# Kernel tuning notes

Hardware: AMD Instinct MI355X
Metric: run time of the kernel (lower is better)

Reference implementation:

```python
import jax, jax.numpy as jnp
import numpy as np

N, E, F, H, ED, C, G = 50000, 800000, 86, 128, 16, 18, 64
NEG_SLOPE = 0.2


def setup_inputs() -> dict:
    key = jax.random.key(0)
    ks = jax.random.split(key, 20)
    s = 0.1
    return {
        "x": jax.random.normal(ks[0], (N, F), jnp.float32),
        "edge_index": jax.random.randint(ks[1], (2, E), 0, N, jnp.int32),
        "edge_attr": jax.random.normal(ks[2], (E, ED), jnp.float32),
        "batch": jnp.sort(jax.random.randint(ks[3], (N,), 0, G, jnp.int32)),
        # conv1 params (GATConv, heads=1): lin, lin_edge (no bias), att vectors, bias
        "W1": jax.random.normal(ks[4], (F, H), jnp.float32) * s,
        "We1": jax.random.normal(ks[5], (ED, H), jnp.float32) * s,
        "as1": jax.random.normal(ks[6], (H,), jnp.float32) * s,
        "ad1": jax.random.normal(ks[7], (H,), jnp.float32) * s,
        "ae1": jax.random.normal(ks[8], (H,), jnp.float32) * s,
        "b1": jnp.zeros((H,), jnp.float32),
        # conv2 params
        "W2": jax.random.normal(ks[9], (H, H), jnp.float32) * s,
        "We2": jax.random.normal(ks[10], (ED, H), jnp.float32) * s,
        "as2": jax.random.normal(ks[11], (H,), jnp.float32) * s,
        "ad2": jax.random.normal(ks[12], (H,), jnp.float32) * s,
        "ae2": jax.random.normal(ks[13], (H,), jnp.float32) * s,
        "b2": jnp.zeros((H,), jnp.float32),
        # final classifier
        "Wl": jax.random.normal(ks[14], (H, C), jnp.float32) * s,
        "bl": jnp.zeros((C,), jnp.float32),
    }


def gat_conv(x, edge_attr, src, dst, W, We, a_src, a_dst, a_edge, bias):
    h = x @ W                                   # [N, H]
    e = edge_attr @ We                          # [E, H]
    # per-edge attention logits: a_src.h_j + a_dst.h_i + a_edge.e
    alpha = (h @ a_src)[src] + (h @ a_dst)[dst] + e @ a_edge   # [E]
    alpha = jax.nn.leaky_relu(alpha, NEG_SLOPE)
    # segment softmax over incoming edges of each destination node
    m = jax.ops.segment_max(alpha, dst, num_segments=N)
    ex = jnp.exp(alpha - m[dst])
    denom = jax.ops.segment_sum(ex, dst, num_segments=N)
    w = ex / jnp.maximum(denom[dst], 1e-16)     # [E]
    out = jax.ops.segment_sum(h[src] * w[:, None], dst, num_segments=N)
    return out + bias


def reference(x, edge_index, edge_attr, batch,
              W1, We1, as1, ad1, ae1, b1,
              W2, We2, as2, ad2, ae2, b2,
              Wl, bl):
    src, dst = edge_index[0], edge_index[1]
    h = jax.nn.relu(gat_conv(x, edge_attr, src, dst, W1, We1, as1, ad1, ae1, b1))
    h = jax.nn.relu(gat_conv(h, edge_attr, src, dst, W2, We2, as2, ad2, ae2, b2))
    pooled = jax.ops.segment_max(h, batch, num_segments=G)      # [G, H] global max pool
    pooled = jnp.where(jnp.isfinite(pooled), pooled, 0.0)       # guard empty graphs
    logits = pooled @ Wl + bl                                   # [G, C]
    return jax.nn.log_softmax(logits, axis=-1)
```

## Files before the change

### kernel.cpp

```cpp
#include <hip/hip_runtime.h>
#include <math.h>

#define N_NODES 50000
#define N_EDGES 800000
#define F_IN    86
#define H_DIM   128
#define ED_DIM  16
#define C_CLS   18
#define G_GRAPHS 64
#define NEG_SLOPE 0.2f
#define SCAN_BLOCKS ((N_NODES + 255) / 256)
#define EB_BLOCKS ((N_EDGES + 255) / 256)
#define GB_BLOCKS ((N_NODES + 63) / 64)
#define HB_BLOCKS 782
#define HB_THREADS (HB_BLOCKS * 256)

typedef _Float16 h2v   __attribute__((ext_vector_type(2)));
typedef _Float16 half8 __attribute__((ext_vector_type(8)));
typedef float    f4v   __attribute__((ext_vector_type(4)));
typedef unsigned long long ull;

__device__ __forceinline__ void atomicMaxFloat(float* addr, float val) {
    if (val >= 0.0f) atomicMax((int*)addr, __float_as_int(val));
    else             atomicMin((unsigned int*)addr, __float_as_uint(val));
}

__global__ void prep(int* __restrict__ cnt, float* __restrict__ pooled,
                     const float* __restrict__ We1, const float* __restrict__ ae1,
                     const float* __restrict__ We2, const float* __restrict__ ae2,
                     float* __restrict__ ve1, float* __restrict__ ve2,
                     const float* __restrict__ W1, const float* __restrict__ W2,
                     _Float16* __restrict__ w1t, _Float16* __restrict__ w2t) {
    int b = blockIdx.x, t = threadIdx.x;
    if (b < SCAN_BLOCKS) {
        int i = b * 256 + t;
        if (i < N_NODES) cnt[i] = 0;
    } else if (b == SCAN_BLOCKS) {
        if (t < ED_DIM) {
            float s = 0.f;
            for (int h = 0; h < H_DIM; ++h) s += We1[t * H_DIM + h] * ae1[h];
            ve1[t] = s;
        } else if (t < 2 * ED_DIM) {
            int j = t - ED_DIM;
            float s = 0.f;
            for (int h = 0; h < H_DIM; ++h) s += We2[j * H_DIM + h] * ae2[h];
            ve2[j] = s;
        }
        for (int i = t; i < G_GRAPHS * H_DIM; i += 256) pooled[i] = 0.f;
    } else if (b == SCAN_BLOCKS + 1) {
        for (int i = t; i < H_DIM * 96; i += 256) {
            int n = i / 96, k = i - n * 96;
            w1t[i] = (k < F_IN) ? (_Float16)W1[k * H_DIM + n] : (_Float16)0.f;
        }
    } else {
        for (int i = t; i < H_DIM * H_DIM; i += 256) {
            int n = i >> 7, k = i & 127;
            w2t[i] = (_Float16)W2[k * H_DIM + n];
        }
    }
}

__global__ void scan1(const int* __restrict__ cnt, int* __restrict__ excl,
                      int* __restrict__ bsum) {
    __shared__ int s[256];
    int tid = threadIdx.x;
    int i = blockIdx.x * 256 + tid;
    int v = (i < N_NODES) ? cnt[i] : 0;
    s[tid] = v;
    __syncthreads();
    for (int o = 1; o < 256; o <<= 1) {
        int t = (tid >= o) ? s[tid - o] : 0;
        __syncthreads();
        s[tid] += t;
        __syncthreads();
    }
    if (i < N_NODES) excl[i] = s[tid] - v;
    if (tid == 255) bsum[blockIdx.x] = s[255];
}

__global__ void scan23(const int* __restrict__ excl, const int* __restrict__ bsum,
                       int* __restrict__ row_ptr) {
    __shared__ int s[256];
    int tid = threadIdx.x;
    int v = (tid < SCAN_BLOCKS) ? bsum[tid] : 0;
    s[tid] = v;
    __syncthreads();
    for (int o = 1; o < 256; o <<= 1) {
        int t = (tid >= o) ? s[tid - o] : 0;
        __syncthreads();
        s[tid] += t;
        __syncthreads();
    }
    int boff = s[blockIdx.x] - bsum[blockIdx.x];
    int i = blockIdx.x * 256 + tid;
    if (i < N_NODES) row_ptr[i] = excl[i] + boff;
    if (i == 0) row_ptr[N_NODES] = N_EDGES;
}

__global__ void scatter_lite(const int* __restrict__ src, const int* __restrict__ dst,
                             const int* __restrict__ row_ptr,
                             const unsigned short* __restrict__ rank,
                             const unsigned int* __restrict__ dotp,
                             int2* __restrict__ perm) {
    int e = blockIdx.x * blockDim.x + threadIdx.x;
    if (e >= N_EDGES) return;
    int pos = row_ptr[dst[e]] + rank[e];
    perm[pos] = make_int2(src[e], (int)dotp[e]);
}

#define KP1 104
__global__ __launch_bounds__(256)
void gemm1_hist(const float* __restrict__ in, const _Float16* __restrict__ w1t,
                const float* __restrict__ a_s, const float* __restrict__ a_d,
                _Float16* __restrict__ hout, float* __restrict__ hs, float* __restrict__ hd,
                const int* __restrict__ dst, int* __restrict__ cnt,
                unsigned short* __restrict__ rank, const float* __restrict__ ea,
                const float* __restrict__ ve1, const float* __restrict__ ve2,
                unsigned int* __restrict__ dotp) {
    __shared__ __attribute__((aligned(16))) _Float16 Asm[64 * KP1];
    __shared__ float sdots[64][2][2];
    int tid = threadIdx.x;

    if (blockIdx.x >= GB_BLOCKS) {
        int tbase = (blockIdx.x - GB_BLOCKS) * 256 + tid;
#pragma unroll
        for (int u = 0; u < 4; ++u) {
            int e = tbase + u * HB_THREADS;
            if (e < N_EDGES) {
                int r = atomicAdd(&cnt[dst[e]], 1);
                rank[e] = (unsigned short)r;
                const float4* p = (const float4*)(ea + (size_t)e * ED_DIM);
                float4 v0 = p[0], v1 = p[1], v2 = p[2], v3 = p[3];
                float s1 = v0.x*ve1[0] + v0.y*ve1[1] + v0.z*ve1[2] + v0.w*ve1[3]
                         + v1.x*ve1[4] + v1.y*ve1[5] + v1.z*ve1[6] + v1.w*ve1[7]
                         + v2.x*ve1[8] + v2.y*ve1[9] + v2.z*ve1[10] + v2.w*ve1[11]
                         + v3.x*ve1[12] + v3.y*ve1[13] + v3.z*ve1[14] + v3.w*ve1[15];
                float s2 = v0.x*ve2[0] + v0.y*ve2[1] + v0.z*ve2[2] + v0.w*ve2[3]
                         + v1.x*ve2[4] + v1.y*ve2[5] + v1.z*ve2[6] + v1.w*ve2[7]
                         + v2.x*ve2[8] + v2.y*ve2[9] + v2.z*ve2[10] + v2.w*ve2[11]
                         + v3.x*ve2[12] + v3.y*ve2[13] + v3.z*ve2[14] + v3.w*ve2[15];
                h2v dv;
                dv.x = (_Float16)s1;
                dv.y = (_Float16)s2;
                dotp[e] = __builtin_bit_cast(unsigned int, dv);
            }
        }
        return;
    }

    int n0 = blockIdx.x * 64;
    const float2* in2 = (const float2*)(in + (size_t)n0 * F_IN);
    for (int idx = tid; idx < 64 * (F_IN / 2); idx += 256) {
        int r = idx / (F_IN / 2), k2 = idx - r * (F_IN / 2);
        float2 v = (n0 + r < N_NODES) ? in2[idx] : make_float2(0.f, 0.f);
        Asm[r * KP1 + 2 * k2]     = (_Float16)v.x;
        Asm[r * KP1 + 2 * k2 + 1] = (_Float16)v.y;
    }
    for (int idx = tid; idx < 64 * (96 - F_IN); idx += 256) {
        int r = idx / (96 - F_IN), k = F_IN + idx - r * (96 - F_IN);
        Asm[r * KP1 + k] = (_Float16)0.f;
    }
    __syncthreads();

    int wave = tid >> 6, lane = tid & 63;
    int wm = (wave & 1) * 32, wn = (wave >> 1) * 64;
    int m16 = lane & 15, quad = lane >> 4;

    f4v acc[2][4];
#pragma unroll
    for (int t = 0; t < 2; ++t)
#pragma unroll
        for (int c = 0; c < 4; ++c) acc[t][c] = (f4v){0.f, 0.f, 0.f, 0.f};

#pragma unroll
    for (int kk = 0; kk < 96 / 32; ++kk) {
        int koff = kk * 32 + quad * 8;
        half8 a0 = *(const half8*)&Asm[(wm + m16) * KP1 + koff];
        half8 a1 = *(const half8*)&Asm[(wm + 16 + m16) * KP1 + koff];
#pragma unroll
        for (int c = 0; c < 4; ++c) {
            half8 b = *(const half8*)&w1t[(wn + c * 16 + m16) * 96 + koff];
            acc[0][c] = __builtin_amdgcn_mfma_f32_16x16x32_f16(a0, b, acc[0][c], 0, 0, 0);
            acc[1][c] = __builtin_amdgcn_mfma_f32_16x16x32_f16(a1, b, acc[1][c], 0, 0, 0);
        }
    }

    float asv[4], adv[4];
#pragma unroll
    for (int c = 0; c < 4; ++c) {
        asv[c] = a_s[wn + c * 16 + m16];
        adv[c] = a_d[wn + c * 16 + m16];
    }
#pragma unroll
    for (int t = 0; t < 2; ++t)
#pragma unroll
        for (int r = 0; r < 4; ++r) {
            float ps = 0.f, pd = 0.f;
#pragma unroll
            for (int c = 0; c < 4; ++c) {
                float v = acc[t][c][r];
                ps += v * asv[c];
                pd += v * adv[c];
            }
#pragma unroll
            for (int o = 1; o < 16; o <<= 1) {
                ps += __shfl_xor(ps, o);
                pd += __shfl_xor(pd, o);
            }
            if (m16 == 0) {
                int row = wm + t * 16 + quad * 4 + r;
                sdots[row][wn >> 6][0] = ps;
                sdots[row][wn >> 6][1] = pd;
            }
        }
#pragma unroll
    for (int t = 0; t < 2; ++t)
#pragma unroll
        for (int c = 0; c < 4; ++c)
#pragma unroll
            for (int r = 0; r < 4; ++r) {
                int row = n0 + wm + t * 16 + quad * 4 + r;
                if (row < N_NODES)
                    hout[(size_t)row * H_DIM + wn + c * 16 + m16] = (_Float16)acc[t][c][r];
            }
    __syncthreads();
    if (tid < 64) {
        int row = n0 + tid;
        if (row < N_NODES) {
            hs[row] = sdots[tid][0][0] + sdots[tid][1][0];
            hd[row] = sdots[tid][0][1] + sdots[tid][1][1];
        }
    }
}

#define KP2 136
__global__ __launch_bounds__(256)
void gemm2(const _Float16* __restrict__ in, const _Float16* __restrict__ w2t,
           const float* __restrict__ a_s, const float* __restrict__ a_d,
           _Float16* __restrict__ hout, float* __restrict__ hs, float* __restrict__ hd) {
    __shared__ __attribute__((aligned(16))) _Float16 Asm[64 * KP2];
    __shared__ float sdots[64][2][2];
    int tid = threadIdx.x;
    int n0 = blockIdx.x * 64;

    const half8* in8 = (const half8*)(in + (size_t)n0 * H_DIM);
    for (int idx = tid; idx < 64 * 16; idx += 256) {
        int r = idx >> 4, k8 = idx & 15;
        half8 v = (n0 + r < N_NODES) ? in8[idx]
                                     : (half8){0, 0, 0, 0, 0, 0, 0, 0};
        *(half8*)&Asm[r * KP2 + k8 * 8] = v;
    }
    __syncthreads();

    int wave = tid >> 6, lane = tid & 63;
    int wm = (wave & 1) * 32, wn = (wave >> 1) * 64;
    int m16 = lane & 15, quad = lane >> 4;

    f4v acc[2][4];
#pragma unroll
    for (int t = 0; t < 2; ++t)
#pragma unroll
        for (int c = 0; c < 4; ++c) acc[t][c] = (f4v){0.f, 0.f, 0.f, 0.f};

#pragma unroll
    for (int kk = 0; kk < 128 / 32; ++kk) {
        int koff = kk * 32 + quad * 8;
        half8 a0 = *(const half8*)&Asm[(wm + m16) * KP2 + koff];
        half8 a1 = *(const half8*)&Asm[(wm + 16 + m16) * KP2 + koff];
#pragma unroll
        for (int c = 0; c < 4; ++c) {
            half8 b = *(const half8*)&w2t[(wn + c * 16 + m16) * H_DIM + koff];
            acc[0][c] = __builtin_amdgcn_mfma_f32_16x16x32_f16(a0, b, acc[0][c], 0, 0, 0);
            acc[1][c] = __builtin_amdgcn_mfma_f32_16x16x32_f16(a1, b, acc[1][c], 0, 0, 0);
        }
    }

    float asv[4], adv[4];
#pragma unroll
    for (int c = 0; c < 4; ++c) {
        asv[c] = a_s[wn + c * 16 + m16];
        adv[c] = a_d[wn + c * 16 + m16];
    }
#pragma unroll
    for (int t = 0; t < 2; ++t)
#pragma unroll
        for (int r = 0; r < 4; ++r) {
            float ps = 0.f, pd = 0.f;
#pragma unroll
            for (int c = 0; c < 4; ++c) {
                float v = acc[t][c][r];
                ps += v * asv[c];
                pd += v * adv[c];
            }
#pragma unroll
            for (int o = 1; o < 16; o <<= 1) {
                ps += __shfl_xor(ps, o);
                pd += __shfl_xor(pd, o);
            }
            if (m16 == 0) {
                int row = wm + t * 16 + quad * 4 + r;
                sdots[row][wn >> 6][0] = ps;
                sdots[row][wn >> 6][1] = pd;
            }
        }
#pragma unroll
    for (int t = 0; t < 2; ++t)
#pragma unroll
        for (int c = 0; c < 4; ++c)
#pragma unroll
            for (int r = 0; r < 4; ++r) {
                int row = n0 + wm + t * 16 + quad * 4 + r;
                if (row < N_NODES)
                    hout[(size_t)row * H_DIM + wn + c * 16 + m16] = (_Float16)acc[t][c][r];
            }
    __syncthreads();
    if (tid < 64) {
        int row = n0 + tid;
        if (row < N_NODES) {
            hs[row] = sdots[tid][0][0] + sdots[tid][1][0];
            hd[row] = sdots[tid][0][1] + sdots[tid][1][1];
        }
    }
}

template<int DOT, bool POOL>
__global__ void gat_node(const int* __restrict__ row_ptr, const int2* __restrict__ perm,
                         const float* __restrict__ hs, const float* __restrict__ hd,
                         const _Float16* __restrict__ h, const float* __restrict__ bias,
                         _Float16* __restrict__ out,
                         const int* __restrict__ batch, float* __restrict__ pooled) {
    __shared__ float smax[H_DIM];
    __shared__ int sg[4];
    __shared__ __attribute__((aligned(16))) ull stage[4][64];
    int tid = threadIdx.x;
    if (POOL) {
        if (tid < H_DIM) smax[tid] = 0.f;
        __syncthreads();
    }
    int n = blockIdx.x * 4 + (tid >> 6);
    int lane = tid & 63;
    int q = lane >> 4, m = lane & 15;
    int r0 = row_ptr[n], r1 = row_ptr[n + 1];
    float hdn = hd[n];
    const char* hb = (const char*)h;
    unsigned mo = (unsigned)(m * 16);
    ull* st = stage[tid >> 6];

    float acc[8];
#pragma unroll
    for (int k = 0; k < 8; ++k) acc[k] = 0.f;
    float denl = 0.f;

    for (int c = r0; c < r1; c += 64) {
        int i = c + lane;
        float w = 0.f;
        int so = 0;
        if (i < r1) {
            int2 p = perm[i];
            so = p.x * (H_DIM * 2);
            h2v dv = __builtin_bit_cast(h2v, p.y);
            float dotv = (DOT == 1) ? (float)dv.x : (float)dv.y;
            float t = hs[p.x] + hdn + dotv;
            t = (t > 0.f) ? t : NEG_SLOPE * t;
            w = __expf(t);
        }
        denl += w;
        st[lane] = (ull)(unsigned)so | ((ull)__float_as_uint(w) << 32);
        int lim = r1 - c; if (lim > 64) lim = 64;
        int njj = (lim + 7) >> 3;
        int jj = 0;
        for (; jj + 2 <= njj; jj += 2) {
            int b8 = jj << 3;
            ull p1 = st[b8 + q];
            ull p2 = st[b8 + q + 4];
            ull p3 = st[b8 + q + 8];
            ull p4 = st[b8 + q + 12];
            float w1 = __uint_as_float((unsigned)(p1 >> 32));
            float w2 = __uint_as_float((unsigned)(p2 >> 32));
            float w3 = __uint_as_float((unsigned)(p3 >> 32));
            float w4 = __uint_as_float((unsigned)(p4 >> 32));
            half8 v1 = *(const half8*)(hb + ((unsigned)p1 + mo));
            half8 v2 = *(const half8*)(hb + ((unsigned)p2 + mo));
            half8 v3 = *(const half8*)(hb + ((unsigned)p3 + mo));
            half8 v4 = *(const half8*)(hb + ((unsigned)p4 + mo));
#pragma unroll
            for (int k = 0; k < 8; ++k) acc[k] += w1 * (float)v1[k];
#pragma unroll
            for (int k = 0; k < 8; ++k) acc[k] += w2 * (float)v2[k];
#pragma unroll
            for (int k = 0; k < 8; ++k) acc[k] += w3 * (float)v3[k];
#pragma unroll
            for (int k = 0; k < 8; ++k) acc[k] += w4 * (float)v4[k];
        }
        if (jj < njj) {
            int b8 = jj << 3;
            ull p1 = st[b8 + q];
            ull p2 = st[b8 + q + 4];
            float w1 = __uint_as_float((unsigned)(p1 >> 32));
            float w2 = __uint_as_float((unsigned)(p2 >> 32));
            half8 v1 = *(const half8*)(hb + ((unsigned)p1 + mo));
            half8 v2 = *(const half8*)(hb + ((unsigned)p2 + mo));
#pragma unroll
            for (int k = 0; k < 8; ++k) acc[k] += w1 * (float)v1[k];
#pragma unroll
            for (int k = 0; k < 8; ++k) acc[k] += w2 * (float)v2[k];
        }
    }
#pragma unroll
    for (int k = 0; k < 8; ++k) {
        acc[k] += __shfl_xor(acc[k], 16);
        acc[k] += __shfl_xor(acc[k], 32);
    }
    float den = denl;
#pragma unroll
    for (int o = 32; o > 0; o >>= 1) den += __shfl_xor(den, o);
    float inv = 1.f / fmaxf(den, 1e-16f);

    float rv[8];
    if (q == 0) {
        float4 b0 = ((const float4*)bias)[2 * m];
        float4 b1 = ((const float4*)bias)[2 * m + 1];
        rv[0] = fmaxf(acc[0] * inv + b0.x, 0.f);
        rv[1] = fmaxf(acc[1] * inv + b0.y, 0.f);
        rv[2] = fmaxf(acc[2] * inv + b0.z, 0.f);
        rv[3] = fmaxf(acc[3] * inv + b0.w, 0.f);
        rv[4] = fmaxf(acc[4] * inv + b1.x, 0.f);
        rv[5] = fmaxf(acc[5] * inv + b1.y, 0.f);
        rv[6] = fmaxf(acc[6] * inv + b1.z, 0.f);
        rv[7] = fmaxf(acc[7] * inv + b1.w, 0.f);
    }

    if (!POOL) {
        if (q == 0) {
            half8 ov;
#pragma unroll
            for (int k = 0; k < 8; ++k) ov[k] = (_Float16)rv[k];
            *(half8*)&out[(size_t)n * H_DIM + m * 8] = ov;
        }
    } else {
        int g = batch[n];
        if (lane == 0) sg[tid >> 6] = g;
        if (q == 0) {
#pragma unroll
            for (int k = 0; k < 8; ++k)
                atomicMax((int*)&smax[m * 8 + k], __float_as_int(rv[k]));
        }
        __syncthreads();
        if (sg[0] == sg[3]) {
            if (tid < H_DIM)
                atomicMaxFloat(&pooled[sg[0] * H_DIM + tid], smax[tid]);
        } else {
            if (q == 0) {
#pragma unroll
                for (int k = 0; k < 8; ++k)
                    atomicMaxFloat(&pooled[g * H_DIM + m * 8 + k], rv[k]);
            }
        }
    }
}

__global__ void final_logits(const float* __restrict__ pooled, const float* __restrict__ Wl,
                             const float* __restrict__ bl, float* __restrict__ outp) {
    int g = threadIdx.x;
    if (g >= G_GRAPHS) return;
    float lg[C_CLS];
#pragma unroll
    for (int c = 0; c < C_CLS; ++c) lg[c] = bl[c];
    for (int k = 0; k < H_DIM; ++k) {
        float v = pooled[g * H_DIM + k];
#pragma unroll
        for (int c = 0; c < C_CLS; ++c) lg[c] += v * Wl[k * C_CLS + c];
    }
    float mx = lg[0];
#pragma unroll
    for (int c = 1; c < C_CLS; ++c) mx = fmaxf(mx, lg[c]);
    float se = 0.f;
#pragma unroll
    for (int c = 0; c < C_CLS; ++c) se += expf(lg[c] - mx);
    float lse = logf(se);
#pragma unroll
    for (int c = 0; c < C_CLS; ++c) outp[g * C_CLS + c] = lg[c] - mx - lse;
}

extern "C" void kernel_launch(void* const* d_in, const int* in_sizes, int n_in,
                              void* d_out, int out_size, void* d_ws, size_t ws_size,
                              hipStream_t stream) {
    const float* x     = (const float*)d_in[0];
    const int*   eidx  = (const int*)d_in[1];
    const float* ea    = (const float*)d_in[2];
    const int*   batch = (const int*)d_in[3];
    const float* W1  = (const float*)d_in[4];
    const float* We1 = (const float*)d_in[5];
    const float* as1 = (const float*)d_in[6];
    const float* ad1 = (const float*)d_in[7];
    const float* ae1 = (const float*)d_in[8];
    const float* b1  = (const float*)d_in[9];
    const float* W2  = (const float*)d_in[10];
    const float* We2 = (const float*)d_in[11];
    const float* as2 = (const float*)d_in[12];
    const float* ad2 = (const float*)d_in[13];
    const float* ae2 = (const float*)d_in[14];
    const float* b2  = (const float*)d_in[15];
    const float* Wl  = (const float*)d_in[16];
    const float* bl  = (const float*)d_in[17];
    float* outp = (float*)d_out;

    const int* src = eidx;
    const int* dst = eidx + N_EDGES;

    char* wsb = (char*)d_ws;
    size_t off = 0;
    auto alloc = [&](size_t bytes) { char* p = wsb + off; off += (bytes + 255) & ~(size_t)255; return p; };
    _Float16* h    = (_Float16*)alloc((size_t)N_NODES * H_DIM * 2);
    _Float16* A2   = (_Float16*)alloc((size_t)N_NODES * H_DIM * 2);
    int2*  perm    = (int2*)alloc((size_t)N_EDGES * 8);
    unsigned short* rank = (unsigned short*)alloc((size_t)N_EDGES * 2);
    unsigned int* dotp = (unsigned int*)alloc((size_t)N_EDGES * 4);
    float* hs      = (float*)alloc(N_NODES * 4);
    float* hd      = (float*)alloc(N_NODES * 4);
    int*   row_ptr = (int*)alloc((N_NODES + 1) * 4);
    int*   cnt     = (int*)alloc(N_NODES * 4);
    int*   excl    = (int*)alloc(N_NODES * 4);
    int*   bsum    = (int*)alloc(SCAN_BLOCKS * 4);
    float* pooled  = (float*)alloc(G_GRAPHS * H_DIM * 4);
    float* ve1     = (float*)alloc(16 * 4);
    float* ve2     = (float*)alloc(16 * 4);
    _Float16* w1t  = (_Float16*)alloc(H_DIM * 96 * 2);
    _Float16* w2t  = (_Float16*)alloc(H_DIM * H_DIM * 2);

    const int NB4 = (N_NODES + 3) / 4;

    prep<<<SCAN_BLOCKS + 3, 256, 0, stream>>>(cnt, pooled, We1, ae1, We2, ae2, ve1, ve2,
                                              W1, W2, w1t, w2t);
    gemm1_hist<<<GB_BLOCKS + HB_BLOCKS, 256, 0, stream>>>(x, w1t, as1, ad1, h, hs, hd,
                                                          dst, cnt, rank, ea, ve1, ve2, dotp);
    scan1<<<SCAN_BLOCKS, 256, 0, stream>>>(cnt, excl, bsum);
    scan23<<<SCAN_BLOCKS, 256, 0, stream>>>(excl, bsum, row_ptr);
    scatter_lite<<<EB_BLOCKS, 256, 0, stream>>>(src, dst, row_ptr, rank, dotp, perm);

    gat_node<1, false><<<NB4, 256, 0, stream>>>(row_ptr, perm, hs, hd, h, b1, A2,
                                                batch, pooled);

    gemm2<<<GB_BLOCKS, 256, 0, stream>>>(A2, w2t, as2, ad2, h, hs, hd);
    gat_node<2, true><<<NB4, 256, 0, stream>>>(row_ptr, perm, hs, hd, h, b2, nullptr,
                                               batch, pooled);

    final_logits<<<1, 64, 0, stream>>>(pooled, Wl, bl, outp);
}
```

Before: 305.6 us.

## Merge edge histogram into GEMM blocks and fuse scan offset with CSR scatter

The edge histogram, rank and edge-attribute dot products are now done inside every GEMM1 block rather than in separate trailing blocks. The atomics are issued early so their latency can overlap the MFMA work, and the weight fragments are hoisted into registers. The second scan pass and the CSR scatter become one kernel that recomputes block offsets in shared memory, which removes a launch and the dependency on row_ptr. In exchange, GEMM blocks carry more register pressure and the scan work is repeated in every one of the 3125 scatter blocks.

After: 310.1 us. No clear change (+1.5%).

```diff
diff --git a/kernel.cpp b/kernel.cpp
--- a/kernel.cpp
+++ b/kernel.cpp
@@ -12,8 +12,7 @@
 #define SCAN_BLOCKS ((N_NODES + 255) / 256)
 #define EB_BLOCKS ((N_EDGES + 255) / 256)
 #define GB_BLOCKS ((N_NODES + 63) / 64)
-#define HB_BLOCKS 782
-#define HB_THREADS (HB_BLOCKS * 256)
+#define HB_THREADS (GB_BLOCKS * 256)
 
 typedef _Float16 h2v   __attribute__((ext_vector_type(2)));
 typedef _Float16 half8 __attribute__((ext_vector_type(8)));
@@ -78,8 +77,12 @@
     if (tid == 255) bsum[blockIdx.x] = s[255];
 }
 
-__global__ void scan23(const int* __restrict__ excl, const int* __restrict__ bsum,
-                       int* __restrict__ row_ptr) {
+__global__ void scan_scatter(const int* __restrict__ excl, const int* __restrict__ bsum,
+                             int* __restrict__ row_ptr,
+                             const int* __restrict__ src, const int* __restrict__ dst,
+                             const unsigned short* __restrict__ rank,
+                             const unsigned int* __restrict__ dotp,
+                             int2* __restrict__ perm) {
     __shared__ int s[256];
     int tid = threadIdx.x;
     int v = (tid < SCAN_BLOCKS) ? bsum[tid] : 0;
@@ -91,21 +94,20 @@
         s[tid] += t;
         __syncthreads();
     }
-    int boff = s[blockIdx.x] - bsum[blockIdx.x];
-    int i = blockIdx.x * 256 + tid;
-    if (i < N_NODES) row_ptr[i] = excl[i] + boff;
-    if (i == 0) row_ptr[N_NODES] = N_EDGES;
-}
-
-__global__ void scatter_lite(const int* __restrict__ src, const int* __restrict__ dst,
-                             const int* __restrict__ row_ptr,
-                             const unsigned short* __restrict__ rank,
-                             const unsigned int* __restrict__ dotp,
-                             int2* __restrict__ perm) {
-    int e = blockIdx.x * blockDim.x + threadIdx.x;
-    if (e >= N_EDGES) return;
-    int pos = row_ptr[dst[e]] + rank[e];
-    perm[pos] = make_int2(src[e], (int)dotp[e]);
+    int eb = s[tid] - v;
+    __syncthreads();
+    s[tid] = eb;
+    __syncthreads();
+    int e = blockIdx.x * 256 + tid;
+    if (blockIdx.x < SCAN_BLOCKS) {
+        if (e < N_NODES) row_ptr[e] = excl[e] + s[e >> 8];
+        if (e == 0) row_ptr[N_NODES] = N_EDGES;
+    }
+    if (e < N_EDGES) {
+        int d = dst[e];
+        int pos = excl[d] + s[d >> 8] + rank[e];
+        perm[pos] = make_int2(src[e], (int)dotp[e]);
+    }
 }
 
 #define KP1 104
@@ -120,35 +122,9 @@
     __shared__ __attribute__((aligned(16))) _Float16 Asm[64 * KP1];
     __shared__ float sdots[64][2][2];
     int tid = threadIdx.x;
-
-    if (blockIdx.x >= GB_BLOCKS) {
-        int tbase = (blockIdx.x - GB_BLOCKS) * 256 + tid;
-#pragma unroll
-        for (int u = 0; u < 4; ++u) {
-            int e = tbase + u * HB_THREADS;
-            if (e < N_EDGES) {
-                int r = atomicAdd(&cnt[dst[e]], 1);
-                rank[e] = (unsigned short)r;
-                const float4* p = (const float4*)(ea + (size_t)e * ED_DIM);
-                float4 v0 = p[0], v1 = p[1], v2 = p[2], v3 = p[3];
-                float s1 = v0.x*ve1[0] + v0.y*ve1[1] + v0.z*ve1[2] + v0.w*ve1[3]
-                         + v1.x*ve1[4] + v1.y*ve1[5] + v1.z*ve1[6] + v1.w*ve1[7]
-                         + v2.x*ve1[8] + v2.y*ve1[9] + v2.z*ve1[10] + v2.w*ve1[11]
-                         + v3.x*ve1[12] + v3.y*ve1[13] + v3.z*ve1[14] + v3.w*ve1[15];
-                float s2 = v0.x*ve2[0] + v0.y*ve2[1] + v0.z*ve2[2] + v0.w*ve2[3]
-                         + v1.x*ve2[4] + v1.y*ve2[5] + v1.z*ve2[6] + v1.w*ve2[7]
-                         + v2.x*ve2[8] + v2.y*ve2[9] + v2.z*ve2[10] + v2.w*ve2[11]
-                         + v3.x*ve2[12] + v3.y*ve2[13] + v3.z*ve2[14] + v3.w*ve2[15];
-                h2v dv;
-                dv.x = (_Float16)s1;
-                dv.y = (_Float16)s2;
-                dotp[e] = __builtin_bit_cast(unsigned int, dv);
-            }
-        }
-        return;
-    }
-
     int n0 = blockIdx.x * 64;
+    int e0 = blockIdx.x * 256 + tid;
+
     const float2* in2 = (const float2*)(in + (size_t)n0 * F_IN);
     for (int idx = tid; idx < 64 * (F_IN / 2); idx += 256) {
         int r = idx / (F_IN / 2), k2 = idx - r * (F_IN / 2);
@@ -166,31 +142,43 @@
     int wm = (wave & 1) * 32, wn = (wave >> 1) * 64;
     int m16 = lane & 15, quad = lane >> 4;
 
+    half8 bf[3][4];
+#pragma unroll
+    for (int kk = 0; kk < 3; ++kk)
+#pragma unroll
+        for (int c = 0; c < 4; ++c)
+            bf[kk][c] = *(const half8*)&w1t[(wn + c * 16 + m16) * 96 + kk * 32 + quad * 8];
+    float asv[4], adv[4];
+#pragma unroll
+    for (int c = 0; c < 4; ++c) {
+        asv[c] = a_s[wn + c * 16 + m16];
+        adv[c] = a_d[wn + c * 16 + m16];
+    }
+
+    int rv4[4];
+#pragma unroll
+    for (int u = 0; u < 4; ++u) {
+        int e = e0 + u * HB_THREADS;
+        rv4[u] = (e < N_EDGES) ? atomicAdd(&cnt[dst[e]], 1) : 0;
+    }
+
     f4v acc[2][4];
 #pragma unroll
     for (int t = 0; t < 2; ++t)
 #pragma unroll
         for (int c = 0; c < 4; ++c) acc[t][c] = (f4v){0.f, 0.f, 0.f, 0.f};
-
-#pragma unroll
-    for (int kk = 0; kk < 96 / 32; ++kk) {
+#pragma unroll
+    for (int kk = 0; kk < 3; ++kk) {
         int koff = kk * 32 + quad * 8;
         half8 a0 = *(const half8*)&Asm[(wm + m16) * KP1 + koff];
         half8 a1 = *(const half8*)&Asm[(wm + 16 + m16) * KP1 + koff];
 #pragma unroll
         for (int c = 0; c < 4; ++c) {
-            half8 b = *(const half8*)&w1t[(wn + c * 16 + m16) * 96 + koff];
-            acc[0][c] = __builtin_amdgcn_mfma_f32_16x16x32_f16(a0, b, acc[0][c], 0, 0, 0);
-            acc[1][c] = __builtin_amdgcn_mfma_f32_16x16x32_f16(a1, b, acc[1][c], 0, 0, 0);
-        }
-    }
-
-    float asv[4], adv[4];
-#pragma unroll
-    for (int c = 0; c < 4; ++c) {
-        asv[c] = a_s[wn + c * 16 + m16];
-        adv[c] = a_d[wn + c * 16 + m16];
-    }
+            acc[0][c] = __builtin_amdgcn_mfma_f32_16x16x32_f16(a0, bf[kk][c], acc[0][c], 0, 0, 0);
+            acc[1][c] = __builtin_amdgcn_mfma_f32_16x16x32_f16(a1, bf[kk][c], acc[1][c], 0, 0, 0);
+        }
+    }
+
 #pragma unroll
     for (int t = 0; t < 2; ++t)
 #pragma unroll
@@ -223,6 +211,28 @@
                 if (row < N_NODES)
                     hout[(size_t)row * H_DIM + wn + c * 16 + m16] = (_Float16)acc[t][c][r];
             }
+
+#pragma unroll
+    for (int u = 0; u < 4; ++u) {
+        int e = e0 + u * HB_THREADS;
+        if (e < N_EDGES) {
+            rank[e] = (unsigned short)rv4[u];
+            const float4* p = (const float4*)(ea + (size_t)e * ED_DIM);
+            float4 v0 = p[0], v1 = p[1], v2 = p[2], v3 = p[3];
+            float s1 = v0.x*ve1[0] + v0.y*ve1[1] + v0.z*ve1[2] + v0.w*ve1[3]
+                     + v1.x*ve1[4] + v1.y*ve1[5] + v1.z*ve1[6] + v1.w*ve1[7]
+                     + v2.x*ve1[8] + v2.y*ve1[9] + v2.z*ve1[10] + v2.w*ve1[11]
+                     + v3.x*ve1[12] + v3.y*ve1[13] + v3.z*ve1[14] + v3.w*ve1[15];
+            float s2 = v0.x*ve2[0] + v0.y*ve2[1] + v0.z*ve2[2] + v0.w*ve2[3]
+                     + v1.x*ve2[4] + v1.y*ve2[5] + v1.z*ve2[6] + v1.w*ve2[7]
+                     + v2.x*ve2[8] + v2.y*ve2[9] + v2.z*ve2[10] + v2.w*ve2[11]
+                     + v3.x*ve2[12] + v3.y*ve2[13] + v3.z*ve2[14] + v3.w*ve2[15];
+            h2v dv;
+            dv.x = (_Float16)s1;
+            dv.y = (_Float16)s2;
+            dotp[e] = __builtin_bit_cast(unsigned int, dv);
+        }
+    }
     __syncthreads();
     if (tid < 64) {
         int row = n0 + tid;
@@ -532,11 +542,11 @@
 
     prep<<<SCAN_BLOCKS + 3, 256, 0, stream>>>(cnt, pooled, We1, ae1, We2, ae2, ve1, ve2,
                                               W1, W2, w1t, w2t);
-    gemm1_hist<<<GB_BLOCKS + HB_BLOCKS, 256, 0, stream>>>(x, w1t, as1, ad1, h, hs, hd,
-                                                          dst, cnt, rank, ea, ve1, ve2, dotp);
+    gemm1_hist<<<GB_BLOCKS, 256, 0, stream>>>(x, w1t, as1, ad1, h, hs, hd,
+                                              dst, cnt, rank, ea, ve1, ve2, dotp);
     scan1<<<SCAN_BLOCKS, 256, 0, stream>>>(cnt, excl, bsum);
-    scan23<<<SCAN_BLOCKS, 256, 0, stream>>>(excl, bsum, row_ptr);
-    scatter_lite<<<EB_BLOCKS, 256, 0, stream>>>(src, dst, row_ptr, rank, dotp, perm);
+    scan_scatter<<<EB_BLOCKS, 256, 0, stream>>>(excl, bsum, row_ptr, src, dst,
+                                                rank, dotp, perm);
 
     gat_node<1, false><<<NB4, 256, 0, stream>>>(row_ptr, perm, hs, hd, h, b1, A2,
                                                 batch, pooled);
```

## Split histogram counters into two banks and fuse scan offsets with edge scatter

Applied to the files above, without the earlier changes.

The per-destination atomic histogram is split into two counter arrays chosen by edge parity, which halves contention on hot counters. The scan-add and scatter kernels are merged into one launch that recomputes block offsets in each block and writes perm directly. The edge-attribute dot products move from the histogram kernel into the scatter, so the dotp intermediate array and its round trip through memory are gone. In exchange, every scatter block redoes the block-sum scan, each edge reads more (excl, cnt0, edge attributes), and an extra counter array must be zeroed and read.

Result: no change. 310.8 us (+1.7%).

```diff
diff --git a/kernel.cpp b/kernel.cpp
--- a/kernel.cpp
+++ b/kernel.cpp
@@ -25,7 +25,8 @@
     else             atomicMin((unsigned int*)addr, __float_as_uint(val));
 }
 
-__global__ void prep(int* __restrict__ cnt, float* __restrict__ pooled,
+__global__ void prep(int* __restrict__ cnt0, int* __restrict__ cnt1,
+                     float* __restrict__ pooled,
                      const float* __restrict__ We1, const float* __restrict__ ae1,
                      const float* __restrict__ We2, const float* __restrict__ ae2,
                      float* __restrict__ ve1, float* __restrict__ ve2,
@@ -34,7 +35,7 @@
     int b = blockIdx.x, t = threadIdx.x;
     if (b < SCAN_BLOCKS) {
         int i = b * 256 + t;
-        if (i < N_NODES) cnt[i] = 0;
+        if (i < N_NODES) { cnt0[i] = 0; cnt1[i] = 0; }
     } else if (b == SCAN_BLOCKS) {
         if (t < ED_DIM) {
             float s = 0.f;
@@ -60,12 +61,12 @@
     }
 }
 
-__global__ void scan1(const int* __restrict__ cnt, int* __restrict__ excl,
-                      int* __restrict__ bsum) {
+__global__ void scan1(const int* __restrict__ cnt0, const int* __restrict__ cnt1,
+                      int* __restrict__ excl, int* __restrict__ bsum) {
     __shared__ int s[256];
     int tid = threadIdx.x;
     int i = blockIdx.x * 256 + tid;
-    int v = (i < N_NODES) ? cnt[i] : 0;
+    int v = (i < N_NODES) ? cnt0[i] + cnt1[i] : 0;
     s[tid] = v;
     __syncthreads();
     for (int o = 1; o < 256; o <<= 1) {
@@ -78,8 +79,14 @@
     if (tid == 255) bsum[blockIdx.x] = s[255];
 }
 
-__global__ void scan23(const int* __restrict__ excl, const int* __restrict__ bsum,
-                       int* __restrict__ row_ptr) {
+__global__ void scan_scatter(const int* __restrict__ excl, const int* __restrict__ bsum,
+                             int* __restrict__ row_ptr,
+                             const int* __restrict__ src, const int* __restrict__ dst,
+                             const unsigned short* __restrict__ rank,
+                             const int* __restrict__ cnt0,
+                             const float* __restrict__ ea,
+                             const float* __restrict__ ve1, const float* __restrict__ ve2,
+                             int2* __restrict__ perm) {
     __shared__ int s[256];
     int tid = threadIdx.x;
     int v = (tid < SCAN_BLOCKS) ? bsum[tid] : 0;
@@ -91,21 +98,35 @@
         s[tid] += t;
         __syncthreads();
     }
-    int boff = s[blockIdx.x] - bsum[blockIdx.x];
-    int i = blockIdx.x * 256 + tid;
-    if (i < N_NODES) row_ptr[i] = excl[i] + boff;
-    if (i == 0) row_ptr[N_NODES] = N_EDGES;
-}
-
-__global__ void scatter_lite(const int* __restrict__ src, const int* __restrict__ dst,
-                             const int* __restrict__ row_ptr,
-                             const unsigned short* __restrict__ rank,
-                             const unsigned int* __restrict__ dotp,
-                             int2* __restrict__ perm) {
-    int e = blockIdx.x * blockDim.x + threadIdx.x;
-    if (e >= N_EDGES) return;
-    int pos = row_ptr[dst[e]] + rank[e];
-    perm[pos] = make_int2(src[e], (int)dotp[e]);
+    int eb = s[tid] - v;
+    __syncthreads();
+    s[tid] = eb;
+    __syncthreads();
+    int e = blockIdx.x * 256 + tid;
+    if (blockIdx.x < SCAN_BLOCKS) {
+        if (e < N_NODES) row_ptr[e] = excl[e] + s[e >> 8];
+        if (e == 0) row_ptr[N_NODES] = N_EDGES;
+    }
+    if (e < N_EDGES) {
+        int d = dst[e];
+        int base = excl[d] + s[d >> 8];
+        int off = (e & 1) ? cnt0[d] : 0;
+        int pos = base + off + rank[e];
+        const float4* p = (const float4*)(ea + (size_t)e * ED_DIM);
+        float4 v0 = p[0], v1 = p[1], v2 = p[2], v3 = p[3];
+        float s1 = v0.x*ve1[0] + v0.y*ve1[1] + v0.z*ve1[2] + v0.w*ve1[3]
+                 + v1.x*ve1[4] + v1.y*ve1[5] + v1.z*ve1[6] + v1.w*ve1[7]
+                 + v2.x*ve1[8] + v2.y*ve1[9] + v2.z*ve1[10] + v2.w*ve1[11]
+                 + v3.x*ve1[12] + v3.y*ve1[13] + v3.z*ve1[14] + v3.w*ve1[15];
+        float s2 = v0.x*ve2[0] + v0.y*ve2[1] + v0.z*ve2[2] + v0.w*ve2[3]
+                 + v1.x*ve2[4] + v1.y*ve2[5] + v1.z*ve2[6] + v1.w*ve2[7]
+                 + v2.x*ve2[8] + v2.y*ve2[9] + v2.z*ve2[10] + v2.w*ve2[11]
+                 + v3.x*ve2[12] + v3.y*ve2[13] + v3.z*ve2[14] + v3.w*ve2[15];
+        h2v dv;
+        dv.x = (_Float16)s1;
+        dv.y = (_Float16)s2;
+        perm[pos] = make_int2(src[e], (int)__builtin_bit_cast(unsigned int, dv));
+    }
 }
 
 #define KP1 104
@@ -113,36 +134,21 @@
 void gemm1_hist(const float* __restrict__ in, const _Float16* __restrict__ w1t,
                 const float* __restrict__ a_s, const float* __restrict__ a_d,
                 _Float16* __restrict__ hout, float* __restrict__ hs, float* __restrict__ hd,
-                const int* __restrict__ dst, int* __restrict__ cnt,
-                unsigned short* __restrict__ rank, const float* __restrict__ ea,
-                const float* __restrict__ ve1, const float* __restrict__ ve2,
-                unsigned int* __restrict__ dotp) {
+                const int* __restrict__ dst, int* __restrict__ cnt0, int* __restrict__ cnt1,
+                unsigned short* __restrict__ rank) {
     __shared__ __attribute__((aligned(16))) _Float16 Asm[64 * KP1];
     __shared__ float sdots[64][2][2];
     int tid = threadIdx.x;
 
     if (blockIdx.x >= GB_BLOCKS) {
         int tbase = (blockIdx.x - GB_BLOCKS) * 256 + tid;
+        int* bank = (tbase & 1) ? cnt1 : cnt0;
 #pragma unroll
         for (int u = 0; u < 4; ++u) {
             int e = tbase + u * HB_THREADS;
             if (e < N_EDGES) {
-                int r = atomicAdd(&cnt[dst[e]], 1);
+                int r = atomicAdd(&bank[dst[e]], 1);
                 rank[e] = (unsigned short)r;
-                const float4* p = (const float4*)(ea + (size_t)e * ED_DIM);
-                float4 v0 = p[0], v1 = p[1], v2 = p[2], v3 = p[3];
-                float s1 = v0.x*ve1[0] + v0.y*ve1[1] + v0.z*ve1[2] + v0.w*ve1[3]
-                         + v1.x*ve1[4] + v1.y*ve1[5] + v1.z*ve1[6] + v1.w*ve1[7]
-                         + v2.x*ve1[8] + v2.y*ve1[9] + v2.z*ve1[10] + v2.w*ve1[11]
-                         + v3.x*ve1[12] + v3.y*ve1[13] + v3.z*ve1[14] + v3.w*ve1[15];
-                float s2 = v0.x*ve2[0] + v0.y*ve2[1] + v0.z*ve2[2] + v0.w*ve2[3]
-                         + v1.x*ve2[4] + v1.y*ve2[5] + v1.z*ve2[6] + v1.w*ve2[7]
-                         + v2.x*ve2[8] + v2.y*ve2[9] + v2.z*ve2[10] + v2.w*ve2[11]
-                         + v3.x*ve2[12] + v3.y*ve2[13] + v3.z*ve2[14] + v3.w*ve2[15];
-                h2v dv;
-                dv.x = (_Float16)s1;
-                dv.y = (_Float16)s2;
-                dotp[e] = __builtin_bit_cast(unsigned int, dv);
             }
         }
         return;
@@ -515,11 +521,11 @@
     _Float16* A2   = (_Float16*)alloc((size_t)N_NODES * H_DIM * 2);
     int2*  perm    = (int2*)alloc((size_t)N_EDGES * 8);
     unsigned short* rank = (unsigned short*)alloc((size_t)N_EDGES * 2);
-    unsigned int* dotp = (unsigned int*)alloc((size_t)N_EDGES * 4);
     float* hs      = (float*)alloc(N_NODES * 4);
     float* hd      = (float*)alloc(N_NODES * 4);
     int*   row_ptr = (int*)alloc((N_NODES + 1) * 4);
-    int*   cnt     = (int*)alloc(N_NODES * 4);
+    int*   cnt0    = (int*)alloc(N_NODES * 4);
+    int*   cnt1    = (int*)alloc(N_NODES * 4);
     int*   excl    = (int*)alloc(N_NODES * 4);
     int*   bsum    = (int*)alloc(SCAN_BLOCKS * 4);
     float* pooled  = (float*)alloc(G_GRAPHS * H_DIM * 4);
@@ -530,13 +536,13 @@
 
     const int NB4 = (N_NODES + 3) / 4;
 
-    prep<<<SCAN_BLOCKS + 3, 256, 0, stream>>>(cnt, pooled, We1, ae1, We2, ae2, ve1, ve2,
-                                              W1, W2, w1t, w2t);
+    prep<<<SCAN_BLOCKS + 3, 256, 0, stream>>>(cnt0, cnt1, pooled, We1, ae1, We2, ae2,
+                                              ve1, ve2, W1, W2, w1t, w2t);
     gemm1_hist<<<GB_BLOCKS + HB_BLOCKS, 256, 0, stream>>>(x, w1t, as1, ad1, h, hs, hd,
-                                                          dst, cnt, rank, ea, ve1, ve2, dotp);
-    scan1<<<SCAN_BLOCKS, 256, 0, stream>>>(cnt, excl, bsum);
-    scan23<<<SCAN_BLOCKS, 256, 0, stream>>>(excl, bsum, row_ptr);
-    scatter_lite<<<EB_BLOCKS, 256, 0, stream>>>(src, dst, row_ptr, rank, dotp, perm);
+                                                          dst, cnt0, cnt1, rank);
+    scan1<<<SCAN_BLOCKS, 256, 0, stream>>>(cnt0, cnt1, excl, bsum);
+    scan_scatter<<<EB_BLOCKS, 256, 0, stream>>>(excl, bsum, row_ptr, src, dst,
+                                                rank, cnt0, ea, ve1, ve2, perm);
 
     gat_node<1, false><<<NB4, 256, 0, stream>>>(row_ptr, perm, hs, hd, h, b1, A2,
                                                 batch, pooled);
```
